# Kernel optimization log

Hardware: AMD Instinct MI355X
Metric: run time of the kernel (lower is better)

Reference implementation:

```python
import jax, jax.numpy as jnp
import numpy as np

IN, HID, NCLS = 16, 50, 20


def setup_inputs() -> dict:
    key = jax.random.key(0)
    ks = jax.random.split(key, 7)
    B, T = 8192, 128
    s_ih = 1.0 / np.sqrt(HID)
    return {
        "x": jax.random.normal(ks[0], (B, T, IN), dtype=jnp.float32),
        # PyTorch LSTM params, gate order (i, f, g, o)
        "W_ih": jax.random.uniform(ks[1], (4 * HID, IN), jnp.float32, -s_ih, s_ih),
        "W_hh": jax.random.uniform(ks[2], (4 * HID, HID), jnp.float32, -s_ih, s_ih),
        "b_ih": jax.random.uniform(ks[3], (4 * HID,), jnp.float32, -s_ih, s_ih),
        "b_hh": jax.random.uniform(ks[4], (4 * HID,), jnp.float32, -s_ih, s_ih),
        "W_fc": jax.random.uniform(ks[5], (NCLS, HID), jnp.float32, -s_ih, s_ih),
        "b_fc": jax.random.uniform(ks[6], (NCLS,), jnp.float32, -s_ih, s_ih),
    }


def _lstm_last_hidden(x, W_ih, W_hh, b_ih, b_hh):
    # x: [B, T, IN] -> precompute input projections for all steps: [T, B, 4H]
    B = x.shape[0]
    xg = jnp.einsum("bti,gi->tbg", x, W_ih) + (b_ih + b_hh)

    def step(carry, xg_t):
        h, c = carry
        gates = xg_t + h @ W_hh.T  # [B, 4H]
        i, f, g, o = jnp.split(gates, 4, axis=-1)
        i = jax.nn.sigmoid(i)
        f = jax.nn.sigmoid(f)
        g = jnp.tanh(g)
        o = jax.nn.sigmoid(o)
        c = f * c + i * g
        h = o * jnp.tanh(c)
        return (h, c), None

    h0 = jnp.zeros((B, HID), x.dtype)
    c0 = jnp.zeros((B, HID), x.dtype)
    (hT, _), _ = jax.lax.scan(step, (h0, c0), xg)
    return hT  # == out[:, -1, :]


def reference(x, W_ih, W_hh, b_ih, b_hh, W_fc, b_fc):
    hT = _lstm_last_hidden(x.astype(jnp.float32), W_ih, W_hh, b_ih, b_hh)
    # dropout is identity in eval mode; relu then linear head on last timestep
    feat = jax.nn.relu(hT)
    logits = feat @ W_fc.T + b_fc  # [B, NCLS]
    return logits
```

## Files before the change

kernel.cpp:

```cpp
#include <hip/hip_runtime.h>

#define IN_    16
#define HID_   50
#define T_     128
#define NCLS_  20
#define BPB_   16
#define NTHR_  512
#define KP_    104
#define KPW_   52

typedef _Float16 half8 __attribute__((ext_vector_type(8)));
typedef float    f32x4 __attribute__((ext_vector_type(4)));
typedef unsigned int u32;

#define L2E_ 1.4426950408889634f
__device__ __forceinline__ u32 pkh2(float a, float b) {
    union { u32 v; _Float16 h[2]; } p; p.h[0] = (_Float16)a; p.h[1] = (_Float16)b; return p.v;
}
#define MFMA(A, B, C) __builtin_amdgcn_mfma_f32_16x16x32_f16((A), (B), (C), 0, 0, 0)
#define SIGS(v)  __builtin_amdgcn_rcpf(1.0f + __builtin_amdgcn_exp2f(v))
#define TANHS(v) fmaf(2.0f, __builtin_amdgcn_rcpf(1.0f + __builtin_amdgcn_exp2f(v)), -1.0f)

__device__ __forceinline__ half8 load_afrag(const float* __restrict__ W_ih,
                                            const float* __restrict__ W_hh,
                                            const float* __restrict__ b_ih,
                                            const float* __restrict__ b_hh,
                                            int s, int c, int q) {
    half8 r = {};
    const int u = s >> 2, kk = s & 3;
    if (u < HID_) {
        const float sc = (kk == 2) ? (-2.0f * L2E_) : (-L2E_);
        const int g = kk * HID_ + u;
        #pragma unroll
        for (int e = 0; e < 8; ++e) {
            const int k = c * 32 + q * 8 + e;
            float w = 0.f;
            if (k < IN_)                 w = W_ih[g * IN_ + k];
            else if (k < IN_ + HID_)     w = W_hh[g * HID_ + (k - IN_)];
            else if (k == IN_ + HID_)    w = b_ih[g] + b_hh[g];
            r[e] = (_Float16)(w * sc);
        }
    }
    return r;
}

__global__ __launch_bounds__(NTHR_, 4)
void lstm_mfma(const float* __restrict__ x,
               const float* __restrict__ W_ih,
               const float* __restrict__ W_hh,
               const float* __restrict__ b_ih,
               const float* __restrict__ b_hh,
               const float* __restrict__ W_fc,
               const float* __restrict__ b_fc,
               float* __restrict__ out)
{
    __shared__ __align__(16) _Float16 st[2][BPB_ * KP_];

    const int tid  = threadIdx.x;
    const int lane = tid & 63;
    const int wv   = tid >> 6;
    const int b0   = blockIdx.x * BPB_;
    const bool comp = (wv < 7);

    for (int idx = tid; idx < 2 * BPB_ * KPW_; idx += NTHR_)
        ((u32*)st)[idx] = ((idx % KPW_) == 33) ? 0x00003C00u : 0u;

    const int q  = lane >> 4;
    const int s0 = 2 * wv * 16 + (lane & 15);
    const int s1 = s0 + 16;
    half8 A00 = {}, A01 = {}, A02 = {}, A10 = {}, A11 = {}, A12 = {};
    if (comp) {
        A00 = load_afrag(W_ih, W_hh, b_ih, b_hh, s0, 0, q);
        A01 = load_afrag(W_ih, W_hh, b_ih, b_hh, s0, 1, q);
        A02 = load_afrag(W_ih, W_hh, b_ih, b_hh, s0, 2, q);
        A10 = load_afrag(W_ih, W_hh, b_ih, b_hh, s1, 0, q);
        A11 = load_afrag(W_ih, W_hh, b_ih, b_hh, s1, 1, q);
        A12 = load_afrag(W_ih, W_hh, b_ih, b_hh, s1, 2, q);
    }
    asm volatile("" : "+v"(A00), "+v"(A01), "+v"(A02),
                      "+v"(A10), "+v"(A11), "+v"(A12));

    const int u0 = 8 * wv + q;
    const int u1 = u0 + 4;
    float c0_ = 0.f, c1_ = 0.f;

    const int bcol  = lane & 15;
    const int brow  = bcol * KP_ + q * 8;
    const int hrow0 = bcol * KP_ + IN_ + u0;
    const int hrow1 = bcol * KP_ + IN_ + u1;

    const int lb = lane >> 2, fq = lane & 3;
    const float* xq = x + (size_t)(b0 + lb) * (T_ * IN_) + 4 * fq;
    const int xo = lb * KPW_ + 2 * fq;

    float4 xr = {0.f, 0.f, 0.f, 0.f};
    __syncthreads();
    if (!comp) {
        const float4 v = *(const float4*)xq;
        u32* d = (u32*)st[0];
        d[xo] = pkh2(v.x, v.y); d[xo + 1] = pkh2(v.z, v.w);
        xr = *(const float4*)(xq + IN_);
    }
    __syncthreads();

    for (int t = 0; t < T_; ++t) {
        const _Float16* sc = st[t & 1];
        _Float16*       sn = st[(t & 1) ^ 1];

        if (comp) {
            const half8 B0 = *(const half8*)(sc + brow);
            const half8 B1 = *(const half8*)(sc + brow + 32);
            const half8 B2 = *(const half8*)(sc + brow + 64);
            const f32x4 Z = {0.f, 0.f, 0.f, 0.f};
            f32x4 C0 = MFMA(A00, B0, Z);
            f32x4 C1 = MFMA(A10, B0, Z);
            C0 = MFMA(A01, B1, C0);
            C1 = MFMA(A11, B1, C1);
            C0 = MFMA(A02, B2, C0);
            C1 = MFMA(A12, B2, C1);

            {
                const float iv = SIGS(C0[0]), fv = SIGS(C0[1]);
                const float gv = TANHS(C0[2]), ov = SIGS(C0[3]);
                c0_ = fmaf(fv, c0_, iv * gv);
                const float hv = ov * TANHS(c0_ * (-2.0f * L2E_));
                if (u0 < HID_) sn[hrow0] = (_Float16)hv;
            }
            {
                const float iv = SIGS(C1[0]), fv = SIGS(C1[1]);
                const float gv = TANHS(C1[2]), ov = SIGS(C1[3]);
                c1_ = fmaf(fv, c1_, iv * gv);
                const float hv = ov * TANHS(c1_ * (-2.0f * L2E_));
                if (u1 < HID_) sn[hrow1] = (_Float16)hv;
            }
        } else {
            if (t + 1 < T_) {
                u32* d = (u32*)sn;
                d[xo] = pkh2(xr.x, xr.y); d[xo + 1] = pkh2(xr.z, xr.w);
            }
            if (t + 2 < T_) xr = *(const float4*)(xq + (size_t)(t + 2) * IN_);
        }
        __syncthreads();
    }

    const _Float16* hf = st[0];

    if (tid < BPB_ * NCLS_) {
        const int b  = tid / NCLS_;
        const int cl = tid - b * NCLS_;
        float acc = b_fc[cl];
        #pragma unroll
        for (int j = 0; j < HID_; ++j) {
            const float hv = fmaxf((float)hf[b * KP_ + IN_ + j], 0.0f);
            acc = fmaf(hv, W_fc[cl * HID_ + j], acc);
        }
        out[(size_t)(b0 + b) * NCLS_ + cl] = acc;
    }
}

extern "C" void kernel_launch(void* const* d_in, const int* in_sizes, int n_in,
                              void* d_out, int out_size, void* d_ws, size_t ws_size,
                              hipStream_t stream) {
    const float* x    = (const float*)d_in[0];
    const float* W_ih = (const float*)d_in[1];
    const float* W_hh = (const float*)d_in[2];
    const float* b_ih = (const float*)d_in[3];
    const float* b_hh = (const float*)d_in[4];
    const float* W_fc = (const float*)d_in[5];
    const float* b_fc = (const float*)d_in[6];
    float* out = (float*)d_out;

    const int B = in_sizes[0] / (T_ * IN_);
    dim3 grid(B / BPB_), block(NTHR_);
    hipLaunchKernelGGL(lstm_mfma, grid, block, 0, stream,
                       x, W_ih, W_hh, b_ih, b_hh, W_fc, b_fc, out);
}
```

Baseline: 100.2 us.

## Shrink block to five waves, give each compute wave three MFMA tiles

Cuts the block from 8 waves to 5 and redistributes the 13 gate tiles: four waves handle three tiles each, and the loader wave also computes the last tile while staging x. Launch bounds rise to 6 blocks per CU. The goal is to remove the idle eighth wave and the underused loader wave, so more blocks fit per CU and barrier cost per block drops. In exchange each compute wave runs a longer serial chain per timestep and needs more registers.

```diff
diff --git a/kernel.cpp b/kernel.cpp
--- a/kernel.cpp
+++ b/kernel.cpp
@@ -5,7 +5,7 @@
 #define T_     128
 #define NCLS_  20
 #define BPB_   16
-#define NTHR_  512
+#define NTHR_  320
 #define KP_    104
 #define KPW_   52
 
@@ -44,7 +44,7 @@
     return r;
 }
 
-__global__ __launch_bounds__(NTHR_, 4)
+__global__ __launch_bounds__(NTHR_, 6)
 void lstm_mfma(const float* __restrict__ x,
                const float* __restrict__ W_ih,
                const float* __restrict__ W_hh,
@@ -60,34 +60,40 @@
     const int lane = tid & 63;
     const int wv   = tid >> 6;
     const int b0   = blockIdx.x * BPB_;
-    const bool comp = (wv < 7);
+    const bool comp = (wv < 4);
 
     for (int idx = tid; idx < 2 * BPB_ * KPW_; idx += NTHR_)
         ((u32*)st)[idx] = ((idx % KPW_) == 33) ? 0x00003C00u : 0u;
 
-    const int q  = lane >> 4;
-    const int s0 = 2 * wv * 16 + (lane & 15);
-    const int s1 = s0 + 16;
-    half8 A00 = {}, A01 = {}, A02 = {}, A10 = {}, A11 = {}, A12 = {};
+    const int q    = lane >> 4;
+    const int bcol = lane & 15;
+    const int brow = bcol * KP_ + q * 8;
+
+    const int t0 = comp ? (3 * wv) : 12;
+    const int s0 = t0 * 16 + (lane & 15);
+    half8 A00 = {}, A01 = {}, A02 = {};
+    half8 A10 = {}, A11 = {}, A12 = {};
+    half8 A20 = {}, A21 = {}, A22 = {};
+    A00 = load_afrag(W_ih, W_hh, b_ih, b_hh, s0, 0, q);
+    A01 = load_afrag(W_ih, W_hh, b_ih, b_hh, s0, 1, q);
+    A02 = load_afrag(W_ih, W_hh, b_ih, b_hh, s0, 2, q);
     if (comp) {
-        A00 = load_afrag(W_ih, W_hh, b_ih, b_hh, s0, 0, q);
-        A01 = load_afrag(W_ih, W_hh, b_ih, b_hh, s0, 1, q);
-        A02 = load_afrag(W_ih, W_hh, b_ih, b_hh, s0, 2, q);
-        A10 = load_afrag(W_ih, W_hh, b_ih, b_hh, s1, 0, q);
-        A11 = load_afrag(W_ih, W_hh, b_ih, b_hh, s1, 1, q);
-        A12 = load_afrag(W_ih, W_hh, b_ih, b_hh, s1, 2, q);
+        A10 = load_afrag(W_ih, W_hh, b_ih, b_hh, s0 + 16, 0, q);
+        A11 = load_afrag(W_ih, W_hh, b_ih, b_hh, s0 + 16, 1, q);
+        A12 = load_afrag(W_ih, W_hh, b_ih, b_hh, s0 + 16, 2, q);
+        A20 = load_afrag(W_ih, W_hh, b_ih, b_hh, s0 + 32, 0, q);
+        A21 = load_afrag(W_ih, W_hh, b_ih, b_hh, s0 + 32, 1, q);
+        A22 = load_afrag(W_ih, W_hh, b_ih, b_hh, s0 + 32, 2, q);
     }
-    asm volatile("" : "+v"(A00), "+v"(A01), "+v"(A02),
-                      "+v"(A10), "+v"(A11), "+v"(A12));
 
-    const int u0 = 8 * wv + q;
+    const int u0 = t0 * 4 + q;
     const int u1 = u0 + 4;
-    float c0_ = 0.f, c1_ = 0.f;
+    const int u2 = u0 + 8;
+    float c0_ = 0.f, c1_ = 0.f, c2_ = 0.f;
 
-    const int bcol  = lane & 15;
-    const int brow  = bcol * KP_ + q * 8;
     const int hrow0 = bcol * KP_ + IN_ + u0;
     const int hrow1 = bcol * KP_ + IN_ + u1;
+    const int hrow2 = bcol * KP_ + IN_ + u2;
 
     const int lb = lane >> 2, fq = lane & 3;
     const float* xq = x + (size_t)(b0 + lb) * (T_ * IN_) + 4 * fq;
@@ -107,33 +113,42 @@
         const _Float16* sc = st[t & 1];
         _Float16*       sn = st[(t & 1) ^ 1];
 
+        const half8 B0 = *(const half8*)(sc + brow);
+        const half8 B1 = *(const half8*)(sc + brow + 32);
+        const half8 B2 = *(const half8*)(sc + brow + 64);
+        const f32x4 Z = {0.f, 0.f, 0.f, 0.f};
+
         if (comp) {
-            const half8 B0 = *(const half8*)(sc + brow);
-            const half8 B1 = *(const half8*)(sc + brow + 32);
-            const half8 B2 = *(const half8*)(sc + brow + 64);
-            const f32x4 Z = {0.f, 0.f, 0.f, 0.f};
             f32x4 C0 = MFMA(A00, B0, Z);
             f32x4 C1 = MFMA(A10, B0, Z);
+            f32x4 C2 = MFMA(A20, B0, Z);
             C0 = MFMA(A01, B1, C0);
             C1 = MFMA(A11, B1, C1);
+            C2 = MFMA(A21, B1, C2);
             C0 = MFMA(A02, B2, C0);
             C1 = MFMA(A12, B2, C1);
+            C2 = MFMA(A22, B2, C2);
 
-            {
-                const float iv = SIGS(C0[0]), fv = SIGS(C0[1]);
+            {   const float iv = SIGS(C0[0]), fv = SIGS(C0[1]);
                 const float gv = TANHS(C0[2]), ov = SIGS(C0[3]);
                 c0_ = fmaf(fv, c0_, iv * gv);
-                const float hv = ov * TANHS(c0_ * (-2.0f * L2E_));
-                if (u0 < HID_) sn[hrow0] = (_Float16)hv;
-            }
-            {
-                const float iv = SIGS(C1[0]), fv = SIGS(C1[1]);
+                sn[hrow0] = (_Float16)(ov * TANHS(c0_ * (-2.0f * L2E_))); }
+            {   const float iv = SIGS(C1[0]), fv = SIGS(C1[1]);
                 const float gv = TANHS(C1[2]), ov = SIGS(C1[3]);
                 c1_ = fmaf(fv, c1_, iv * gv);
-                const float hv = ov * TANHS(c1_ * (-2.0f * L2E_));
-                if (u1 < HID_) sn[hrow1] = (_Float16)hv;
-            }
+                sn[hrow1] = (_Float16)(ov * TANHS(c1_ * (-2.0f * L2E_))); }
+            {   const float iv = SIGS(C2[0]), fv = SIGS(C2[1]);
+                const float gv = TANHS(C2[2]), ov = SIGS(C2[3]);
+                c2_ = fmaf(fv, c2_, iv * gv);
+                sn[hrow2] = (_Float16)(ov * TANHS(c2_ * (-2.0f * L2E_))); }
         } else {
+            f32x4 C0 = MFMA(A00, B0, Z);
+            C0 = MFMA(A01, B1, C0);
+            C0 = MFMA(A02, B2, C0);
+            const float iv = SIGS(C0[0]), fv = SIGS(C0[1]);
+            const float gv = TANHS(C0[2]), ov = SIGS(C0[3]);
+            c0_ = fmaf(fv, c0_, iv * gv);
+            if (u0 < HID_) sn[hrow0] = (_Float16)(ov * TANHS(c0_ * (-2.0f * L2E_)));
             if (t + 1 < T_) {
                 u32* d = (u32*)sn;
                 d[xo] = pkh2(xr.x, xr.y); d[xo + 1] = pkh2(xr.z, xr.w);
@@ -145,7 +160,7 @@
 
     const _Float16* hf = st[0];
 
-    if (tid < BPB_ * NCLS_) {
+    {
         const int b  = tid / NCLS_;
         const int cl = tid - b * NCLS_;
         float acc = b_fc[cl];
```

New measurement: 92.39 us. -7.8%, faster.
